# Kernel tuning notes

Hardware: AMD Instinct MI355X
Metric: run time of the kernel (lower is better)

## Reference

```python
import jax, jax.numpy as jnp
import numpy as np

B, Q, K, D_IN, H, D_V = 4, 1024, 1024, 256, 64, 128
MASK_VAL = -1000000.0


def setup_inputs() -> dict:
    key = jax.random.key(0)
    k1, k2, k3, k4, k5, k6, k7 = jax.random.split(key, 7)
    queries = jax.random.normal(k1, (B, Q, D_IN), dtype=jnp.float32)
    keys = jax.random.normal(k2, (B, K, D_IN), dtype=jnp.float32)
    values = jax.random.normal(k3, (B, K, D_V), dtype=jnp.float32)
    valid_lens = jax.random.randint(k4, (B,), 1, K + 1)
    # Linear weights (no bias), stored as (in, out) for direct matmul
    W_q = jax.random.normal(k5, (D_IN, H), dtype=jnp.float32) / np.sqrt(D_IN)
    W_k = jax.random.normal(k6, (D_IN, H), dtype=jnp.float32) / np.sqrt(D_IN)
    w_v = jax.random.normal(k7, (H,), dtype=jnp.float32) / np.sqrt(H)
    return {"queries": queries, "keys": keys, "values": values,
            "valid_lens": valid_lens, "W_q": W_q, "W_k": W_k, "w_v": w_v}


def reference(queries, keys, values, valid_lens, W_q, W_k, w_v):
    # Project queries and keys to hidden dim H
    q = jnp.einsum("bqd,dh->bqh", queries, W_q)   # (B, Q, H)
    k = jnp.einsum("bkd,dh->bkh", keys, W_k)      # (B, K, H)
    # Additive (Bahdanau) scoring: broadcast-add + tanh + reduce over H
    feats = jnp.tanh(q[:, :, None, :] + k[:, None, :, :])   # (B, Q, K, H)
    scores = jnp.einsum("bqkh,h->bqk", feats, w_v)           # (B, Q, K)
    # Masked softmax over keys: positions >= valid_len get -1e6
    key_pos = jnp.arange(scores.shape[-1])                    # (K,)
    mask = key_pos[None, None, :] >= valid_lens[:, None, None]
    scores = jnp.where(mask, MASK_VAL, scores)
    attn = jax.nn.softmax(scores, axis=-1)                    # (B, Q, K)
    # Weighted sum of values (dropout is identity at rate 0.0 / eval)
    return jnp.einsum("bqk,bkv->bqv", attn, values)           # (B, Q, D_V)
```

## Files before the change

kernel.cpp:

```cpp
#include <hip/hip_runtime.h>
#include <hip/hip_fp16.h>
#include <math.h>

#define B_ 4
#define Q_ 1024
#define K_ 1024
#define DIN_ 256
#define H_ 64
#define DV_ 128
#define KT 64
#define MASKV -1000000.0f
#define C2LOG2E 2.8853900817779268f
#define LOG2E 1.4426950408889634f

__device__ __forceinline__ float fexp2(float x) {
#if __has_builtin(__builtin_amdgcn_exp2f)
  return __builtin_amdgcn_exp2f(x);
#else
  return exp2f(x);
#endif
}
__device__ __forceinline__ float frcp(float x) {
#if __has_builtin(__builtin_amdgcn_rcpf)
  return __builtin_amdgcn_rcpf(x);
#else
  return 1.0f / x;
#endif
}

__global__ __launch_bounds__(256, 4) void prep_kernel(
    const float* __restrict__ queries, const float* __restrict__ keys,
    const float* __restrict__ values,
    const float* __restrict__ Wq, const float* __restrict__ Wk,
    float* __restrict__ eq, float* __restrict__ ek,
    unsigned short* __restrict__ vh) {
  int bid = blockIdx.x;
  int t = threadIdx.x;
  if (bid >= 512) {
    int i = ((bid - 512) * 256 + t) * 4;
    float4 v = *(const float4*)&values[i];
    ushort4 o;
    o.x = __half_as_ushort(__float2half(v.x));
    o.y = __half_as_ushort(__float2half(v.y));
    o.z = __half_as_ushort(__float2half(v.z));
    o.w = __half_as_ushort(__float2half(v.w));
    *(ushort4*)&vh[i] = o;
    return;
  }
  int w = t >> 6, lane = t & 63;
  int r0 = __builtin_amdgcn_readfirstlane(bid * 16 + w * 4);
  const float* src;
  const float* W;
  float* dst;
  if (r0 < B_ * Q_) {
    src = queries + r0 * DIN_; W = Wq; dst = eq + r0 * H_;
  } else {
    int kr = r0 - B_ * Q_;
    src = keys + kr * DIN_; W = Wk; dst = ek + kr * H_;
  }
  float a00 = 0.f, a01 = 0.f, a10 = 0.f, a11 = 0.f;
  float a20 = 0.f, a21 = 0.f, a30 = 0.f, a31 = 0.f;
#pragma unroll 8
  for (int d = 0; d < DIN_; d += 2) {
    float w0 = W[d * H_ + lane];
    float w1 = W[(d + 1) * H_ + lane];
    a00 = fmaf(w0, src[d], a00);             a01 = fmaf(w1, src[d + 1], a01);
    a10 = fmaf(w0, src[DIN_ + d], a10);      a11 = fmaf(w1, src[DIN_ + d + 1], a11);
    a20 = fmaf(w0, src[2 * DIN_ + d], a20);  a21 = fmaf(w1, src[2 * DIN_ + d + 1], a21);
    a30 = fmaf(w0, src[3 * DIN_ + d], a30);  a31 = fmaf(w1, src[3 * DIN_ + d + 1], a31);
  }
  dst[lane]          = fexp2((a00 + a01) * C2LOG2E);
  dst[H_ + lane]     = fexp2((a10 + a11) * C2LOG2E);
  dst[2 * H_ + lane] = fexp2((a20 + a21) * C2LOG2E);
  dst[3 * H_ + lane] = fexp2((a30 + a31) * C2LOG2E);
}

__global__ __launch_bounds__(256, 4) void attn_kernel(
    const float* __restrict__ eq, const float* __restrict__ ek,
    const unsigned* __restrict__ vh32, const float* __restrict__ wv,
    const int* __restrict__ vlen,
    float* __restrict__ pml, float* __restrict__ po,
    int ns, int span) {
  __shared__ __align__(16) float ek_s[KT][H_ + 4];
  __shared__ __align__(16) unsigned v_s[KT][DV_ / 2];
  __shared__ __align__(16) float p_s[4][2][KT];
  int t = threadIdx.x;
  int lane = t & 63;
  int w = t >> 6;
  int bid = blockIdx.x;
  int s = blockIdx.y;
  int b = bid >> 7;
  int q0 = __builtin_amdgcn_readfirstlane(((bid & 127) * 4 + w) * 2);
  int kv = vlen[b];
  int g = b * Q_ + q0;
  int k_lo = s * span;

  if (k_lo >= kv) {
    if (lane == 0) {
      *(float2*)&pml[(g * ns + s) * 2] = make_float2(-1e38f, 0.f);
      *(float2*)&pml[((g + 1) * ns + s) * 2] = make_float2(-1e38f, 0.f);
    }
    return;
  }

  const float* eqa = eq + (long)g * H_;
  const float* eqb = eqa + H_;
  const float* ekb = ek + b * K_ * H_;

  float wsum = wv[lane];
#pragma unroll
  for (int sh = 32; sh >= 1; sh >>= 1) wsum += __shfl_xor(wsum, sh);

  float ma = -1e38f, mb = -1e38f, la = 0.f, lb = 0.f;
  float oa0 = 0.f, oa1 = 0.f, ob0 = 0.f, ob1 = 0.f;
  int tile0 = k_lo >> 6;
  int tileE = min((kv + KT - 1) >> 6, (k_lo + span) >> 6);

  for (int tile = tile0; tile < tileE; ++tile) {
    int k0 = tile * KT;

    __syncthreads();
    {
      const float4* gek = (const float4*)(ekb + (size_t)k0 * H_);
      const float4* gv = (const float4*)(vh32 + (size_t)(b * K_ + k0) * (DV_ / 2));
#pragma unroll
      for (int i = 0; i < 4; ++i) {
        int f4 = i * 256 + t;
        *(float4*)&ek_s[f4 >> 4][(f4 & 15) * 4] = gek[f4];
      }
#pragma unroll
      for (int i = 0; i < 4; ++i) {
        int f4 = i * 256 + t;
        *(float4*)&v_s[f4 >> 4][(f4 & 15) * 4] = gv[f4];
      }
    }
    __syncthreads();

    const float* ekrow = ek_s[lane];
    float aa0 = 0.f, aa1 = 0.f, ab0 = 0.f, ab1 = 0.f;
#pragma unroll
    for (int h4 = 0; h4 < H_ / 4; ++h4) {
      float4 e4 = *(const float4*)&ekrow[h4 * 4];
#pragma unroll
      for (int j = 0; j < 4; ++j) {
        int h = h4 * 4 + j;
        float ekv = (j == 0) ? e4.x : (j == 1) ? e4.y : (j == 2) ? e4.z : e4.w;
        float wvh = wv[h];
        float ra = frcp(fmaf(ekv, eqa[h], 1.0f));
        float rb = frcp(fmaf(ekv, eqb[h], 1.0f));
        if (j & 1) { aa1 = fmaf(wvh, ra, aa1); ab1 = fmaf(wvh, rb, ab1); }
        else       { aa0 = fmaf(wvh, ra, aa0); ab0 = fmaf(wvh, rb, ab0); }
      }
    }
    float xa = fmaf(-2.f, aa0 + aa1, wsum);
    float xb = fmaf(-2.f, ab0 + ab1, wsum);
    if (k0 + lane >= kv) { xa = MASKV; xb = MASKV; }

    float mta = xa, mtb = xb;
#pragma unroll
    for (int sh = 32; sh >= 1; sh >>= 1) {
      mta = fmaxf(mta, __shfl_xor(mta, sh));
      mtb = fmaxf(mtb, __shfl_xor(mtb, sh));
    }
    float mna = fmaxf(ma, mta), mnb = fmaxf(mb, mtb);
    float pa = fexp2((xa - mna) * LOG2E);
    float pb = fexp2((xb - mnb) * LOG2E);
    float psa = pa, psb = pb;
#pragma unroll
    for (int sh = 32; sh >= 1; sh >>= 1) {
      psa += __shfl_xor(psa, sh);
      psb += __shfl_xor(psb, sh);
    }
    float sca = fexp2((ma - mna) * LOG2E);
    float scb = fexp2((mb - mnb) * LOG2E);
    la = fmaf(la, sca, psa); lb = fmaf(lb, scb, psb);
    ma = mna; mb = mnb;
    oa0 *= sca; oa1 *= sca; ob0 *= scb; ob1 *= scb;
    p_s[w][0][lane] = pa;
    p_s[w][1][lane] = pb;

#pragma unroll 4
    for (int k4 = 0; k4 < KT / 4; ++k4) {
      float4 pa4 = *(const float4*)&p_s[w][0][k4 * 4];
      float4 pb4 = *(const float4*)&p_s[w][1][k4 * 4];
      unsigned u0 = v_s[k4 * 4 + 0][lane];
      unsigned u1 = v_s[k4 * 4 + 1][lane];
      unsigned u2 = v_s[k4 * 4 + 2][lane];
      unsigned u3 = v_s[k4 * 4 + 3][lane];
      __half2 h0 = *(__half2*)&u0, h1 = *(__half2*)&u1;
      __half2 h2 = *(__half2*)&u2, h3 = *(__half2*)&u3;
      float v00 = __low2float(h0), v01 = __high2float(h0);
      float v10 = __low2float(h1), v11 = __high2float(h1);
      float v20 = __low2float(h2), v21 = __high2float(h2);
      float v30 = __low2float(h3), v31 = __high2float(h3);
      oa0 = fmaf(pa4.x, v00, oa0); oa1 = fmaf(pa4.x, v01, oa1);
      ob0 = fmaf(pb4.x, v00, ob0); ob1 = fmaf(pb4.x, v01, ob1);
      oa0 = fmaf(pa4.y, v10, oa0); oa1 = fmaf(pa4.y, v11, oa1);
      ob0 = fmaf(pb4.y, v10, ob0); ob1 = fmaf(pb4.y, v11, ob1);
      oa0 = fmaf(pa4.z, v20, oa0); oa1 = fmaf(pa4.z, v21, oa1);
      ob0 = fmaf(pb4.z, v20, ob0); ob1 = fmaf(pb4.z, v21, ob1);
      oa0 = fmaf(pa4.w, v30, oa0); oa1 = fmaf(pa4.w, v31, oa1);
      ob0 = fmaf(pb4.w, v30, ob0); ob1 = fmaf(pb4.w, v31, ob1);
    }
  }

  long pbase = ((long)g * ns + s) * DV_ + lane * 2;
  *(float2*)&po[pbase] = make_float2(oa0, oa1);
  *(float2*)&po[pbase + (long)ns * DV_] = make_float2(ob0, ob1);
  if (lane == 0) {
    *(float2*)&pml[(g * ns + s) * 2] = make_float2(ma, la);
    *(float2*)&pml[((g + 1) * ns + s) * 2] = make_float2(mb, lb);
  }
}

__global__ __launch_bounds__(256, 4) void combine_kernel(
    const float* __restrict__ pml, const float* __restrict__ po,
    float* __restrict__ out, int ns) {
  int t = threadIdx.x;
  int lane = t & 63;
  int w = t >> 6;
  int qrow = blockIdx.x * 4 + w;
  float M = -1e38f;
  for (int s = 0; s < ns; ++s) {
    float2 v = *(const float2*)&pml[(qrow * ns + s) * 2];
    M = fmaxf(M, v.x);
  }
  float L = 0.f, ax = 0.f, ay = 0.f;
  for (int s = 0; s < ns; ++s) {
    float2 v = *(const float2*)&pml[(qrow * ns + s) * 2];
    if (v.y > 0.f) {
      float wgt = fexp2((v.x - M) * LOG2E);
      L = fmaf(v.y, wgt, L);
      float2 o2 = *(const float2*)&po[((long)qrow * ns + s) * DV_ + lane * 2];
      ax = fmaf(o2.x, wgt, ax);
      ay = fmaf(o2.y, wgt, ay);
    }
  }
  float inv = frcp(L);
  *(float2*)&out[(long)qrow * DV_ + lane * 2] = make_float2(ax * inv, ay * inv);
}

extern "C" void kernel_launch(void* const* d_in, const int* in_sizes, int n_in,
                              void* d_out, int out_size, void* d_ws, size_t ws_size,
                              hipStream_t stream) {
  const float* queries = (const float*)d_in[0];
  const float* keys    = (const float*)d_in[1];
  const float* values  = (const float*)d_in[2];
  const int*   vl      = (const int*)d_in[3];
  const float* Wq      = (const float*)d_in[4];
  const float* Wk      = (const float*)d_in[5];
  const float* wv      = (const float*)d_in[6];
  float* out = (float*)d_out;

  float* eq = (float*)d_ws;
  float* ek = eq + (size_t)B_ * Q_ * H_;
  unsigned short* vh = (unsigned short*)(ek + (size_t)B_ * K_ * H_);
  char* dyn = (char*)(vh + (size_t)B_ * K_ * DV_);
  size_t fixed = (size_t)(dyn - (char*)d_ws);

  int ns = 2;
  for (int cand = 8; cand >= 2; cand >>= 1) {
    size_t need = fixed + (size_t)B_ * Q_ * cand * 8
                + (size_t)B_ * Q_ * cand * DV_ * 4;
    if (ws_size >= need) { ns = cand; break; }
  }
  int span = K_ / ns;
  float* pml = (float*)dyn;
  float* po = pml + (size_t)B_ * Q_ * ns * 2;

  prep_kernel<<<dim3(1024), dim3(256), 0, stream>>>(
      queries, keys, values, Wq, Wk, eq, ek, vh);
  attn_kernel<<<dim3(B_ * (Q_ / 8), ns), dim3(256), 0, stream>>>(
      eq, ek, (const unsigned*)vh, wv, vl, pml, po, ns, span);
  combine_kernel<<<dim3(B_ * Q_ / 4), dim3(256), 0, stream>>>(pml, po, out, ns);
}
```

Measured before the change: 47.28 us.

## Drop online-softmax max tracking, pair reciprocals, raise queries per wave, prefetch tiles

Uses the bound on the tanh-based scores (at most sum|w_v|) to drop the running max and rescaling, so partials hold only sums and combine adds them directly. Pairs two reciprocals into one via a common denominator. Each wave now handles four query rows instead of two, reusing K/V tiles across more queries. It also prefetches the next K/V tile into registers, and the split count is fixed at four. The risks are higher register pressure and possible precision or overflow issues from the unstabilized exp and the product denominators.

```diff
diff --git a/kernel.cpp b/kernel.cpp
--- a/kernel.cpp
+++ b/kernel.cpp
@@ -9,7 +9,10 @@
 #define H_ 64
 #define DV_ 128
 #define KT 64
-#define MASKV -1000000.0f
+#define NS 4
+#define SPAN 256
+#define GQ 4
+#define MASKP -1000000.0f
 #define C2LOG2E 2.8853900817779268f
 #define LOG2E 1.4426950408889634f
 
@@ -79,165 +82,200 @@
     const float* __restrict__ eq, const float* __restrict__ ek,
     const unsigned* __restrict__ vh32, const float* __restrict__ wv,
     const int* __restrict__ vlen,
-    float* __restrict__ pml, float* __restrict__ po,
-    int ns, int span) {
+    float* __restrict__ pl, float* __restrict__ po) {
   __shared__ __align__(16) float ek_s[KT][H_ + 4];
   __shared__ __align__(16) unsigned v_s[KT][DV_ / 2];
-  __shared__ __align__(16) float p_s[4][2][KT];
+  __shared__ __align__(16) float p_s[4][GQ][KT];
   int t = threadIdx.x;
   int lane = t & 63;
   int w = t >> 6;
-  int bid = blockIdx.x;
+  int b = blockIdx.x >> 6;
+  int qt = blockIdx.x & 63;
   int s = blockIdx.y;
-  int b = bid >> 7;
-  int q0 = __builtin_amdgcn_readfirstlane(((bid & 127) * 4 + w) * 2);
+  int q0 = __builtin_amdgcn_readfirstlane(qt * 16 + w * GQ);
   int kv = vlen[b];
   int g = b * Q_ + q0;
-  int k_lo = s * span;
+  int k_lo = s * SPAN;
 
   if (k_lo >= kv) {
     if (lane == 0) {
-      *(float2*)&pml[(g * ns + s) * 2] = make_float2(-1e38f, 0.f);
-      *(float2*)&pml[((g + 1) * ns + s) * 2] = make_float2(-1e38f, 0.f);
+#pragma unroll
+      for (int i = 0; i < GQ; ++i) pl[(g + i) * NS + s] = 0.f;
     }
     return;
   }
 
-  const float* eqa = eq + (long)g * H_;
-  const float* eqb = eqa + H_;
-  const float* ekb = ek + b * K_ * H_;
+  const float* eq0 = eq + (size_t)g * H_;
+  const float* eq1 = eq0 + H_;
+  const float* eq2 = eq0 + 2 * H_;
+  const float* eq3 = eq0 + 3 * H_;
+  const float* ekb = ek + (size_t)b * K_ * H_;
+  const unsigned* vgb = vh32 + (size_t)b * K_ * (DV_ / 2);
 
   float wsum = wv[lane];
 #pragma unroll
   for (int sh = 32; sh >= 1; sh >>= 1) wsum += __shfl_xor(wsum, sh);
-
-  float ma = -1e38f, mb = -1e38f, la = 0.f, lb = 0.f;
-  float oa0 = 0.f, oa1 = 0.f, ob0 = 0.f, ob1 = 0.f;
+  float wl2 = wsum * LOG2E;
+  const float nl2 = -2.0f * LOG2E;
+
+  float l0 = 0.f, l1 = 0.f, l2 = 0.f, l3 = 0.f;
+  float o0x = 0.f, o0y = 0.f, o1x = 0.f, o1y = 0.f;
+  float o2x = 0.f, o2y = 0.f, o3x = 0.f, o3y = 0.f;
+
   int tile0 = k_lo >> 6;
-  int tileE = min((kv + KT - 1) >> 6, (k_lo + span) >> 6);
-
+  int tileE = min((kv + KT - 1) >> 6, tile0 + SPAN / KT);
+
+  float4 reb0, reb1, reb2, reb3, rvb0, rvb1, rvb2, rvb3;
+  auto issue = [&](int tile) {
+    const float4* gek = (const float4*)(ekb + (size_t)(tile * KT) * H_);
+    const float4* gv = (const float4*)(vgb + (size_t)(tile * KT) * (DV_ / 2));
+    reb0 = gek[t]; reb1 = gek[256 + t]; reb2 = gek[512 + t]; reb3 = gek[768 + t];
+    rvb0 = gv[t];  rvb1 = gv[256 + t];  rvb2 = gv[512 + t];  rvb3 = gv[768 + t];
+  };
+  auto store_lds = [&]() {
+    int f4 = t;
+    *(float4*)&ek_s[f4 >> 4][(f4 & 15) * 4] = reb0;
+    *(float4*)&v_s[f4 >> 4][(f4 & 15) * 4] = rvb0;
+    f4 = 256 + t;
+    *(float4*)&ek_s[f4 >> 4][(f4 & 15) * 4] = reb1;
+    *(float4*)&v_s[f4 >> 4][(f4 & 15) * 4] = rvb1;
+    f4 = 512 + t;
+    *(float4*)&ek_s[f4 >> 4][(f4 & 15) * 4] = reb2;
+    *(float4*)&v_s[f4 >> 4][(f4 & 15) * 4] = rvb2;
+    f4 = 768 + t;
+    *(float4*)&ek_s[f4 >> 4][(f4 & 15) * 4] = reb3;
+    *(float4*)&v_s[f4 >> 4][(f4 & 15) * 4] = rvb3;
+  };
+
+  issue(tile0);
   for (int tile = tile0; tile < tileE; ++tile) {
     int k0 = tile * KT;
-
     __syncthreads();
-    {
-      const float4* gek = (const float4*)(ekb + (size_t)k0 * H_);
-      const float4* gv = (const float4*)(vh32 + (size_t)(b * K_ + k0) * (DV_ / 2));
-#pragma unroll
-      for (int i = 0; i < 4; ++i) {
-        int f4 = i * 256 + t;
-        *(float4*)&ek_s[f4 >> 4][(f4 & 15) * 4] = gek[f4];
+    store_lds();
+    if (tile + 1 < tileE) issue(tile + 1);
+    __syncthreads();
+
+    const float* ekrow = ek_s[lane];
+    float acc0 = 0.f, acc1 = 0.f, acc2 = 0.f, acc3 = 0.f;
+#pragma unroll
+    for (int hp = 0; hp < H_ / 2; ++hp) {
+      int h = hp * 2;
+      float ek0 = ekrow[h], ek1 = ekrow[h + 1];
+      float w0 = wv[h], w1 = wv[h + 1];
+      {
+        float E0 = eq0[h] * ek0, E1 = eq0[h + 1] * ek1;
+        float d0 = 1.f + E0, d1 = 1.f + E1;
+        float num = fmaf(w1, d0, w0 * d1);
+        acc0 = fmaf(num, frcp(d0 * d1), acc0);
       }
-#pragma unroll
-      for (int i = 0; i < 4; ++i) {
-        int f4 = i * 256 + t;
-        *(float4*)&v_s[f4 >> 4][(f4 & 15) * 4] = gv[f4];
+      {
+        float E0 = eq1[h] * ek0, E1 = eq1[h + 1] * ek1;
+        float d0 = 1.f + E0, d1 = 1.f + E1;
+        float num = fmaf(w1, d0, w0 * d1);
+        acc1 = fmaf(num, frcp(d0 * d1), acc1);
+      }
+      {
+        float E0 = eq2[h] * ek0, E1 = eq2[h + 1] * ek1;
+        float d0 = 1.f + E0, d1 = 1.f + E1;
+        float num = fmaf(w1, d0, w0 * d1);
+        acc2 = fmaf(num, frcp(d0 * d1), acc2);
+      }
+      {
+        float E0 = eq3[h] * ek0, E1 = eq3[h + 1] * ek1;
+        float d0 = 1.f + E0, d1 = 1.f + E1;
+        float num = fmaf(w1, d0, w0 * d1);
+        acc3 = fmaf(num, frcp(d0 * d1), acc3);
       }
     }
-    __syncthreads();
-
-    const float* ekrow = ek_s[lane];
-    float aa0 = 0.f, aa1 = 0.f, ab0 = 0.f, ab1 = 0.f;
-#pragma unroll
-    for (int h4 = 0; h4 < H_ / 4; ++h4) {
-      float4 e4 = *(const float4*)&ekrow[h4 * 4];
-#pragma unroll
-      for (int j = 0; j < 4; ++j) {
-        int h = h4 * 4 + j;
-        float ekv = (j == 0) ? e4.x : (j == 1) ? e4.y : (j == 2) ? e4.z : e4.w;
-        float wvh = wv[h];
-        float ra = frcp(fmaf(ekv, eqa[h], 1.0f));
-        float rb = frcp(fmaf(ekv, eqb[h], 1.0f));
-        if (j & 1) { aa1 = fmaf(wvh, ra, aa1); ab1 = fmaf(wvh, rb, ab1); }
-        else       { aa0 = fmaf(wvh, ra, aa0); ab0 = fmaf(wvh, rb, ab0); }
-      }
-    }
-    float xa = fmaf(-2.f, aa0 + aa1, wsum);
-    float xb = fmaf(-2.f, ab0 + ab1, wsum);
-    if (k0 + lane >= kv) { xa = MASKV; xb = MASKV; }
-
-    float mta = xa, mtb = xb;
-#pragma unroll
-    for (int sh = 32; sh >= 1; sh >>= 1) {
-      mta = fmaxf(mta, __shfl_xor(mta, sh));
-      mtb = fmaxf(mtb, __shfl_xor(mtb, sh));
-    }
-    float mna = fmaxf(ma, mta), mnb = fmaxf(mb, mtb);
-    float pa = fexp2((xa - mna) * LOG2E);
-    float pb = fexp2((xb - mnb) * LOG2E);
-    float psa = pa, psb = pb;
-#pragma unroll
-    for (int sh = 32; sh >= 1; sh >>= 1) {
-      psa += __shfl_xor(psa, sh);
-      psb += __shfl_xor(psb, sh);
-    }
-    float sca = fexp2((ma - mna) * LOG2E);
-    float scb = fexp2((mb - mnb) * LOG2E);
-    la = fmaf(la, sca, psa); lb = fmaf(lb, scb, psb);
-    ma = mna; mb = mnb;
-    oa0 *= sca; oa1 *= sca; ob0 *= scb; ob1 *= scb;
-    p_s[w][0][lane] = pa;
-    p_s[w][1][lane] = pb;
+    bool maskd = (k0 + lane) >= kv;
+    float t0 = fmaf(nl2, acc0, wl2);
+    float t1 = fmaf(nl2, acc1, wl2);
+    float t2 = fmaf(nl2, acc2, wl2);
+    float t3 = fmaf(nl2, acc3, wl2);
+    if (maskd) { t0 = MASKP; t1 = MASKP; t2 = MASKP; t3 = MASKP; }
+    float p0 = fexp2(t0), p1 = fexp2(t1), p2 = fexp2(t2), p3 = fexp2(t3);
+    l0 += p0; l1 += p1; l2 += p2; l3 += p3;
+    p_s[w][0][lane] = p0;
+    p_s[w][1][lane] = p1;
+    p_s[w][2][lane] = p2;
+    p_s[w][3][lane] = p3;
 
 #pragma unroll 4
     for (int k4 = 0; k4 < KT / 4; ++k4) {
-      float4 pa4 = *(const float4*)&p_s[w][0][k4 * 4];
-      float4 pb4 = *(const float4*)&p_s[w][1][k4 * 4];
-      unsigned u0 = v_s[k4 * 4 + 0][lane];
-      unsigned u1 = v_s[k4 * 4 + 1][lane];
-      unsigned u2 = v_s[k4 * 4 + 2][lane];
-      unsigned u3 = v_s[k4 * 4 + 3][lane];
+      int kk = k4 * 4;
+      float4 P0 = *(const float4*)&p_s[w][0][kk];
+      float4 P1 = *(const float4*)&p_s[w][1][kk];
+      float4 P2 = *(const float4*)&p_s[w][2][kk];
+      float4 P3 = *(const float4*)&p_s[w][3][kk];
+      unsigned u0 = v_s[kk][lane];
+      unsigned u1 = v_s[kk + 1][lane];
+      unsigned u2 = v_s[kk + 2][lane];
+      unsigned u3 = v_s[kk + 3][lane];
       __half2 h0 = *(__half2*)&u0, h1 = *(__half2*)&u1;
       __half2 h2 = *(__half2*)&u2, h3 = *(__half2*)&u3;
-      float v00 = __low2float(h0), v01 = __high2float(h0);
-      float v10 = __low2float(h1), v11 = __high2float(h1);
-      float v20 = __low2float(h2), v21 = __high2float(h2);
-      float v30 = __low2float(h3), v31 = __high2float(h3);
-      oa0 = fmaf(pa4.x, v00, oa0); oa1 = fmaf(pa4.x, v01, oa1);
-      ob0 = fmaf(pb4.x, v00, ob0); ob1 = fmaf(pb4.x, v01, ob1);
-      oa0 = fmaf(pa4.y, v10, oa0); oa1 = fmaf(pa4.y, v11, oa1);
-      ob0 = fmaf(pb4.y, v10, ob0); ob1 = fmaf(pb4.y, v11, ob1);
-      oa0 = fmaf(pa4.z, v20, oa0); oa1 = fmaf(pa4.z, v21, oa1);
-      ob0 = fmaf(pb4.z, v20, ob0); ob1 = fmaf(pb4.z, v21, ob1);
-      oa0 = fmaf(pa4.w, v30, oa0); oa1 = fmaf(pa4.w, v31, oa1);
-      ob0 = fmaf(pb4.w, v30, ob0); ob1 = fmaf(pb4.w, v31, ob1);
+      float v0x = __low2float(h0), v0y = __high2float(h0);
+      float v1x = __low2float(h1), v1y = __high2float(h1);
+      float v2x = __low2float(h2), v2y = __high2float(h2);
+      float v3x = __low2float(h3), v3y = __high2float(h3);
+      o0x = fmaf(P0.x, v0x, o0x); o0y = fmaf(P0.x, v0y, o0y);
+      o1x = fmaf(P1.x, v0x, o1x); o1y = fmaf(P1.x, v0y, o1y);
+      o2x = fmaf(P2.x, v0x, o2x); o2y = fmaf(P2.x, v0y, o2y);
+      o3x = fmaf(P3.x, v0x, o3x); o3y = fmaf(P3.x, v0y, o3y);
+      o0x = fmaf(P0.y, v1x, o0x); o0y = fmaf(P0.y, v1y, o0y);
+      o1x = fmaf(P1.y, v1x, o1x); o1y = fmaf(P1.y, v1y, o1y);
+      o2x = fmaf(P2.y, v1x, o2x); o2y = fmaf(P2.y, v1y, o2y);
+      o3x = fmaf(P3.y, v1x, o3x); o3y = fmaf(P3.y, v1y, o3y);
+      o0x = fmaf(P0.z, v2x, o0x); o0y = fmaf(P0.z, v2y, o0y);
+      o1x = fmaf(P1.z, v2x, o1x); o1y = fmaf(P1.z, v2y, o1y);
+      o2x = fmaf(P2.z, v2x, o2x); o2y = fmaf(P2.z, v2y, o2y);
+      o3x = fmaf(P3.z, v2x, o3x); o3y = fmaf(P3.z, v2y, o3y);
+      o0x = fmaf(P0.w, v3x, o0x); o0y = fmaf(P0.w, v3y, o0y);
+      o1x = fmaf(P1.w, v3x, o1x); o1y = fmaf(P1.w, v3y, o1y);
+      o2x = fmaf(P2.w, v3x, o2x); o2y = fmaf(P2.w, v3y, o2y);
+      o3x = fmaf(P3.w, v3x, o3x); o3y = fmaf(P3.w, v3y, o3y);
     }
   }
 
-  long pbase = ((long)g * ns + s) * DV_ + lane * 2;
-  *(float2*)&po[pbase] = make_float2(oa0, oa1);
-  *(float2*)&po[pbase + (long)ns * DV_] = make_float2(ob0, ob1);
+#pragma unroll
+  for (int sh = 32; sh >= 1; sh >>= 1) {
+    l0 += __shfl_xor(l0, sh);
+    l1 += __shfl_xor(l1, sh);
+    l2 += __shfl_xor(l2, sh);
+    l3 += __shfl_xor(l3, sh);
+  }
   if (lane == 0) {
-    *(float2*)&pml[(g * ns + s) * 2] = make_float2(ma, la);
-    *(float2*)&pml[((g + 1) * ns + s) * 2] = make_float2(mb, lb);
-  }
+    pl[(g + 0) * NS + s] = l0;
+    pl[(g + 1) * NS + s] = l1;
+    pl[(g + 2) * NS + s] = l2;
+    pl[(g + 3) * NS + s] = l3;
+  }
+  size_t pb = ((size_t)g * NS + s) * DV_ + lane * 2;
+  *(float2*)&po[pb] = make_float2(o0x, o0y);
+  *(float2*)&po[pb + (size_t)NS * DV_] = make_float2(o1x, o1y);
+  *(float2*)&po[pb + (size_t)2 * NS * DV_] = make_float2(o2x, o2y);
+  *(float2*)&po[pb + (size_t)3 * NS * DV_] = make_float2(o3x, o3y);
 }
 
 __global__ __launch_bounds__(256, 4) void combine_kernel(
-    const float* __restrict__ pml, const float* __restrict__ po,
-    float* __restrict__ out, int ns) {
+    const float* __restrict__ pl, const float* __restrict__ po,
+    float* __restrict__ out) {
   int t = threadIdx.x;
   int lane = t & 63;
   int w = t >> 6;
-  int qrow = blockIdx.x * 4 + w;
-  float M = -1e38f;
-  for (int s = 0; s < ns; ++s) {
-    float2 v = *(const float2*)&pml[(qrow * ns + s) * 2];
-    M = fmaxf(M, v.x);
-  }
+  int g = blockIdx.x * 4 + w;
   float L = 0.f, ax = 0.f, ay = 0.f;
-  for (int s = 0; s < ns; ++s) {
-    float2 v = *(const float2*)&pml[(qrow * ns + s) * 2];
-    if (v.y > 0.f) {
-      float wgt = fexp2((v.x - M) * LOG2E);
-      L = fmaf(v.y, wgt, L);
-      float2 o2 = *(const float2*)&po[((long)qrow * ns + s) * DV_ + lane * 2];
-      ax = fmaf(o2.x, wgt, ax);
-      ay = fmaf(o2.y, wgt, ay);
+#pragma unroll
+  for (int s = 0; s < NS; ++s) {
+    float ls = pl[g * NS + s];
+    if (ls != 0.f) {
+      L += ls;
+      float2 o2 = *(const float2*)&po[((size_t)g * NS + s) * DV_ + lane * 2];
+      ax += o2.x;
+      ay += o2.y;
     }
   }
   float inv = frcp(L);
-  *(float2*)&out[(long)qrow * DV_ + lane * 2] = make_float2(ax * inv, ay * inv);
+  *(float2*)&out[(size_t)g * DV_ + lane * 2] = make_float2(ax * inv, ay * inv);
 }
 
 extern "C" void kernel_launch(void* const* d_in, const int* in_sizes, int n_in,
@@ -255,22 +293,12 @@
   float* eq = (float*)d_ws;
   float* ek = eq + (size_t)B_ * Q_ * H_;
   unsigned short* vh = (unsigned short*)(ek + (size_t)B_ * K_ * H_);
-  char* dyn = (char*)(vh + (size_t)B_ * K_ * DV_);
-  size_t fixed = (size_t)(dyn - (char*)d_ws);
-
-  int ns = 2;
-  for (int cand = 8; cand >= 2; cand >>= 1) {
-    size_t need = fixed + (size_t)B_ * Q_ * cand * 8
-                + (size_t)B_ * Q_ * cand * DV_ * 4;
-    if (ws_size >= need) { ns = cand; break; }
-  }
-  int span = K_ / ns;
-  float* pml = (float*)dyn;
-  float* po = pml + (size_t)B_ * Q_ * ns * 2;
+  float* pl = (float*)(vh + (size_t)B_ * K_ * DV_);
+  float* po = pl + (size_t)B_ * Q_ * NS;
 
   prep_kernel<<<dim3(1024), dim3(256), 0, stream>>>(
       queries, keys, values, Wq, Wk, eq, ek, vh);
-  attn_kernel<<<dim3(B_ * (Q_ / 8), ns), dim3(256), 0, stream>>>(
-      eq, ek, (const unsigned*)vh, wv, vl, pml, po, ns, span);
-  combine_kernel<<<dim3(B_ * Q_ / 4), dim3(256), 0, stream>>>(pml, po, out, ns);
-}
+  attn_kernel<<<dim3(B_ * (Q_ / 16), NS), dim3(256), 0, stream>>>(
+      eq, ek, (const unsigned*)vh, wv, vl, pl, po);
+  combine_kernel<<<dim3(B_ * Q_ / 4), dim3(256), 0, stream>>>(pl, po, out);
+}
```

Result: slower. 49.24 us (+4.2%).
